# Performance work log

Hardware: AMD Instinct MI355X
Metric: run time of the kernel (lower is better)

## Reference

```python
import jax, jax.numpy as jnp
import numpy as np

# dims: B=4 batch, S=2048 seq, D=4096 in, O=4096 out, E=16 adapters, R=16 rank

def setup_inputs() -> dict:
    key = jax.random.key(0)
    k = jax.random.split(key, 6)
    x = jax.random.normal(k[0], (4, 2048, 4096), jnp.float32)
    W = jax.random.normal(k[1], (4096, 4096), jnp.float32) * 0.02   # base_linear.weight [O, D]
    bias = jax.random.normal(k[2], (4096,), jnp.float32) * 0.02
    A = jax.random.normal(k[3], (16, 16, 4096), jnp.float32) * 0.02  # stacked a_factors [E, R, D]
    Bf = jax.random.normal(k[4], (16, 4096, 16), jnp.float32) * 0.02 # stacked b_factors [E, O, R]
    coeffs = jax.random.uniform(k[5], (16,), jnp.float32)            # task coefficients per adapter
    scales = jnp.full((16,), 0.5, jnp.float32)                       # per-adapter static scales
    return {"x": x, "W": W, "bias": bias, "A": A, "Bf": Bf, "coeffs": coeffs, "scales": scales}

def reference(x, W, bias, A, Bf, coeffs, scales):
    # base: out = x @ W.T + bias
    out = jnp.einsum('bsd,od->bso', x, W) + bias
    # fused LoRA: sum_e coeffs[e]*scales[e] * (x @ A[e].T) @ Bf[e].T
    xa = jnp.einsum('bsd,erd->ebsr', x, A)          # [E, B, S, R] (small: R=16)
    w = coeffs * scales                               # [E]
    upd = jnp.einsum('ebsr,eor,e->bso', xa, Bf, w)  # weighted accumulate over adapters
    return out + upd
```

## Files before the change

### kernel.cpp

```cpp
#include <hip/hip_runtime.h>

typedef float f32x4 __attribute__((ext_vector_type(4)));
typedef __bf16 bf16x8 __attribute__((ext_vector_type(8)));
typedef unsigned short u16x8 __attribute__((ext_vector_type(8)));

__device__ __forceinline__ unsigned short f2bf(float f) {
  union { float f; unsigned int u; } v; v.f = f;
  unsigned int u = v.u;
  unsigned int r = (u + 0x7FFFu + ((u >> 16) & 1u)) >> 16;
  return (unsigned short)r;
}

__global__ __launch_bounds__(256) void k_cast_bf16(const float* __restrict__ in,
                                                   unsigned short* __restrict__ out, int n8) {
  const f32x4* p = (const f32x4*)in;
  for (int i = blockIdx.x * 256 + threadIdx.x; i < n8; i += 2048 * 256) {
    f32x4 a = p[2 * i], b = p[2 * i + 1];
    u16x8 o;
    o[0] = f2bf(a[0]); o[1] = f2bf(a[1]); o[2] = f2bf(a[2]); o[3] = f2bf(a[3]);
    o[4] = f2bf(b[0]); o[5] = f2bf(b[1]); o[6] = f2bf(b[2]); o[7] = f2bf(b[3]);
    ((u16x8*)out)[i] = o;
  }
}

__global__ void k_build_bw(const float* __restrict__ Bf,
                           const float* __restrict__ coeffs,
                           const float* __restrict__ scales,
                           unsigned short* __restrict__ bw) {
  int t = blockIdx.x * 256 + threadIdx.x;
  int o = t >> 8, k = t & 255, e = k >> 4, r = k & 15;
  float v = coeffs[e] * scales[e] * Bf[((size_t)e * 4096 + o) * 16 + r];
  bw[t] = f2bf(v);
}

__global__ void k_build_at(const float* __restrict__ A,
                           unsigned short* __restrict__ at) {
  __shared__ float tile[64][65];
  int kt = blockIdx.x * 64, dt = blockIdx.y * 64;
  int tx = threadIdx.x & 63, ty = threadIdx.x >> 6;
#pragma unroll
  for (int j = 0; j < 64; j += 4)
    tile[ty + j][tx] = A[(size_t)(kt + ty + j) * 4096 + dt + tx];
  __syncthreads();
#pragma unroll
  for (int j = 0; j < 64; j += 4)
    at[(size_t)(dt + ty + j) * 256 + kt + tx] = f2bf(tile[tx][ty + j]);
}

template <int M_, int N_, int K_>
__global__ __launch_bounds__(256) void k_gemm_prep(
    const unsigned short* __restrict__ Abuf,
    const unsigned short* __restrict__ Bbuf,
    const float* __restrict__ Wadd,
    unsigned short* __restrict__ outB) {
  constexpr int NBN = N_ / 128;
  constexpr int NWG = (M_ / 128) * NBN;
  const int bid = blockIdx.x;
  const int swz = (bid & 7) * (NWG / 8) + (bid >> 3);
  const int bm = swz / NBN, bn = swz % NBN;

  __shared__ unsigned short ldsA[128 * 64];
  __shared__ unsigned short ldsB[128 * 64];

  const int t = threadIdx.x, w = t >> 6, l = t & 63;
  const int wr = w >> 1, wc = w & 1;

  f32x4 acc[4][4] = {};
  const int m0 = bm * 128, n0 = bn * 128;
  const int srow = w * 8 + (l >> 3);
  const int scol = (l & 7) * 8;
  const unsigned short* gA = Abuf + (size_t)(m0 + srow) * K_ + scol;
  const unsigned short* gB = Bbuf + (size_t)(n0 + srow) * K_ + scol;

  for (int kt = 0; kt < K_; kt += 64) {
#pragma unroll
    for (int i = 0; i < 4; ++i) {
      __builtin_amdgcn_global_load_lds(
          (__attribute__((address_space(1))) void*)(gA + (size_t)i * 32 * K_ + kt),
          (__attribute__((address_space(3))) void*)(ldsA + i * 2048 + w * 512), 16, 0, 0);
      __builtin_amdgcn_global_load_lds(
          (__attribute__((address_space(1))) void*)(gB + (size_t)i * 32 * K_ + kt),
          (__attribute__((address_space(3))) void*)(ldsB + i * 2048 + w * 512), 16, 0, 0);
    }
    __syncthreads();
#pragma unroll
    for (int kk = 0; kk < 2; ++kk) {
      const int col = kk * 32 + (l >> 4) * 8;
      const int arow = wr * 64 + (l & 15);
      const int brow = wc * 64 + (l & 15);
      bf16x8 af[4], bfv[4];
#pragma unroll
      for (int mi = 0; mi < 4; ++mi)
        af[mi] = *(const bf16x8*)&ldsA[(arow + mi * 16) * 64 + col];
#pragma unroll
      for (int ni = 0; ni < 4; ++ni)
        bfv[ni] = *(const bf16x8*)&ldsB[(brow + ni * 16) * 64 + col];
#pragma unroll
      for (int mi = 0; mi < 4; ++mi)
#pragma unroll
        for (int ni = 0; ni < 4; ++ni)
          acc[mi][ni] = __builtin_amdgcn_mfma_f32_16x16x32_bf16(
              af[mi], bfv[ni], acc[mi][ni], 0, 0, 0);
    }
    __syncthreads();
  }

  const int mrow0 = m0 + wr * 64 + (l >> 4) * 4;
  const int ncol0 = n0 + wc * 64 + (l & 15);
#pragma unroll
  for (int mi = 0; mi < 4; ++mi)
#pragma unroll
    for (int r = 0; r < 4; ++r) {
      const int m = mrow0 + mi * 16 + r;
#pragma unroll
      for (int ni = 0; ni < 4; ++ni) {
        const int n = ncol0 + ni * 16;
        outB[(size_t)m * N_ + n] = f2bf(acc[mi][ni][r] + Wadd[(size_t)m * N_ + n]);
      }
    }
}

template <int M_, int N_, int K_>
__global__ __launch_bounds__(512, 2) void k_gemm256(
    const unsigned short* __restrict__ Abuf,
    const unsigned short* __restrict__ Bbuf,
    const float* __restrict__ bias,
    float* __restrict__ outF) {
  constexpr int NBN = N_ / 256;
  constexpr int NWG = (M_ / 256) * NBN;
  constexpr int NT = K_ / 32;
  static_assert(NWG % 8 == 0, "bijective xcd swizzle");
  static_assert(NT >= 4, "pipeline depth");

  const int bid = blockIdx.x;
  const int swz = (bid & 7) * (NWG / 8) + (bid >> 3);
  const int bm = swz / NBN, bn = swz % NBN;
  const int m0 = bm * 256, n0 = bn * 256;

  __shared__ __attribute__((aligned(128))) unsigned short lds[65536];
  char* ldsb = (char*)lds;

  const int tid = threadIdx.x, w = tid >> 6, l = tid & 63;
  const int wr = w >> 2, wc = w & 3;

  const int scol = ((l & 3) ^ ((l >> 3) & 3)) * 8;
  const unsigned short* gA = Abuf + (size_t)(m0 + w * 16 + (l >> 2)) * K_ + scol;
  const unsigned short* gB = Bbuf + (size_t)(n0 + w * 16 + (l >> 2)) * K_ + scol;
  const int dA = w * 1024;
  const int dB = 16384 + w * 1024;

  const int qp = ((l >> 4) ^ ((l >> 1) & 3)) << 4;
  const int raOff = (wr * 128 + (l & 15)) * 64 + qp;
  const int rbOff = 16384 + (wc * 64 + (l & 15)) * 64 + qp;

  f32x4 acc[8][4] = {};

#define STAGE_A(tt)                                                                   \
  do {                                                                                \
    const int bb_ = ((tt) & 3) << 15;                                                 \
    const size_t ko_ = (size_t)(tt) * 32;                                             \
    _Pragma("unroll") for (int i_ = 0; i_ < 2; ++i_) {                                \
      __builtin_amdgcn_global_load_lds(                                               \
          (__attribute__((address_space(1))) void*)(gA + (size_t)i_ * 128 * K_ + ko_),\
          (__attribute__((address_space(3))) void*)(ldsb + bb_ + i_ * 8192 + dA),     \
          16, 0, 0);                                                                  \
    }                                                                                 \
  } while (0)
#define STAGE_B(tt)                                                                   \
  do {                                                                                \
    const int bb_ = ((tt) & 3) << 15;                                                 \
    const size_t ko_ = (size_t)(tt) * 32;                                             \
    _Pragma("unroll") for (int i_ = 0; i_ < 2; ++i_) {                                \
      __builtin_amdgcn_global_load_lds(                                               \
          (__attribute__((address_space(1))) void*)(gB + (size_t)i_ * 128 * K_ + ko_),\
          (__attribute__((address_space(3))) void*)(ldsb + bb_ + i_ * 8192 + dB),     \
          16, 0, 0);                                                                  \
    }                                                                                 \
  } while (0)

  STAGE_A(0); STAGE_B(0); STAGE_A(1); STAGE_B(1); STAGE_A(2); STAGE_B(2);

  for (int t = 0; t < NT; ++t) {
    const int bb0 = (t & 3) << 15;

    if (t + 3 < NT) STAGE_A(t + 3);
    if (t + 3 < NT)      asm volatile("s_waitcnt vmcnt(10)" ::: "memory");
    else if (t + 2 < NT) asm volatile("s_waitcnt vmcnt(8)" ::: "memory");
    else if (t + 1 < NT) asm volatile("s_waitcnt vmcnt(4)" ::: "memory");
    else                 asm volatile("s_waitcnt vmcnt(0)" ::: "memory");
    __builtin_amdgcn_s_barrier();
    __builtin_amdgcn_sched_barrier(0);

    bf16x8 af[4], bv[4];
#pragma unroll
    for (int mi = 0; mi < 4; ++mi)
      af[mi] = *(const bf16x8*)(ldsb + bb0 + raOff + mi * 1024);
#pragma unroll
    for (int ni = 0; ni < 4; ++ni)
      bv[ni] = *(const bf16x8*)(ldsb + bb0 + rbOff + ni * 1024);

    __builtin_amdgcn_s_barrier();
    __builtin_amdgcn_sched_barrier(0);
    __builtin_amdgcn_s_setprio(1);
#pragma unroll
    for (int mi = 0; mi < 4; ++mi)
#pragma unroll
      for (int ni = 0; ni < 4; ++ni)
        acc[mi][ni] = __builtin_amdgcn_mfma_f32_16x16x32_bf16(
            af[mi], bv[ni], acc[mi][ni], 0, 0, 0);
    __builtin_amdgcn_s_setprio(0);

    if (t + 3 < NT) STAGE_B(t + 3);
    bf16x8 ag[4];
#pragma unroll
    for (int mi = 0; mi < 4; ++mi)
      ag[mi] = *(const bf16x8*)(ldsb + bb0 + raOff + (mi + 4) * 1024);

    __builtin_amdgcn_s_barrier();
    __builtin_amdgcn_sched_barrier(0);
    __builtin_amdgcn_s_setprio(1);
#pragma unroll
    for (int mi = 0; mi < 4; ++mi)
#pragma unroll
      for (int ni = 0; ni < 4; ++ni)
        acc[mi + 4][ni] = __builtin_amdgcn_mfma_f32_16x16x32_bf16(
            ag[mi], bv[ni], acc[mi + 4][ni], 0, 0, 0);
    __builtin_amdgcn_s_setprio(0);
  }
#undef STAGE_A
#undef STAGE_B

#pragma unroll
  for (int ni = 0; ni < 4; ++ni) {
    const int n = n0 + wc * 64 + ni * 16 + (l & 15);
    const float bv2 = bias[n];
#pragma unroll
    for (int mi = 0; mi < 8; ++mi) {
      const int m = m0 + wr * 128 + mi * 16 + (l >> 4) * 4;
#pragma unroll
      for (int r = 0; r < 4; ++r)
        outF[(size_t)(m + r) * N_ + n] = acc[mi][ni][r] + bv2;
    }
  }
}

extern "C" void kernel_launch(void* const* d_in, const int* in_sizes, int n_in,
                              void* d_out, int out_size, void* d_ws, size_t ws_size,
                              hipStream_t stream) {
  const float* x      = (const float*)d_in[0];
  const float* W      = (const float*)d_in[1];
  const float* bias   = (const float*)d_in[2];
  const float* A      = (const float*)d_in[3];
  const float* Bf     = (const float*)d_in[4];
  const float* coeffs = (const float*)d_in[5];
  const float* scales = (const float*)d_in[6];
  float* out = (float*)d_out;

  char* ws = (char*)d_ws;
  unsigned short* xb   = (unsigned short*)(ws);
  unsigned short* weff = (unsigned short*)(ws + 67108864);
  unsigned short* bw   = (unsigned short*)(ws + 67108864 + 33554432);
  unsigned short* at   = (unsigned short*)(ws + 67108864 + 33554432 + 2097152);

  k_cast_bf16<<<2048, 256, 0, stream>>>(x, xb, (8192 * 4096) / 8);
  k_build_bw<<<4096, 256, 0, stream>>>(Bf, coeffs, scales, bw);
  k_build_at<<<dim3(4, 64), 256, 0, stream>>>(A, at);
  k_gemm_prep<4096, 4096, 256><<<1024, 256, 0, stream>>>(bw, at, W, weff);
  k_gemm256<8192, 4096, 4096><<<512, 512, 0, stream>>>(xb, weff, bias, out);
}
```

Measured before the change: 359.6 us.

## Unroll GEMM k-loop by two with a five-slot LDS ring buffer

Replaces the four-slot LDS ring with a five-slot ring and processes two k-tiles per loop iteration. This allows a single barrier per pair of k-steps instead of two barriers per step. A and B stages are merged into one load macro, and LDS fragment reads for the next tile are interleaved with MFMA blocks. The aim is to cut barrier and synchronisation overhead and to improve overlap of LDS reads with matrix math. The cost is more LDS (160KB), higher register pressure from holding two tiles of fragments, and an extra requirement that NT be even.

```diff
diff --git a/kernel.cpp b/kernel.cpp
--- a/kernel.cpp
+++ b/kernel.cpp
@@ -130,14 +130,14 @@
   constexpr int NWG = (M_ / 256) * NBN;
   constexpr int NT = K_ / 32;
   static_assert(NWG % 8 == 0, "bijective xcd swizzle");
-  static_assert(NT >= 4, "pipeline depth");
+  static_assert(NT % 2 == 0 && NT >= 6, "pipeline depth");
 
   const int bid = blockIdx.x;
   const int swz = (bid & 7) * (NWG / 8) + (bid >> 3);
   const int bm = swz / NBN, bn = swz % NBN;
   const int m0 = bm * 256, n0 = bn * 256;
 
-  __shared__ __attribute__((aligned(128))) unsigned short lds[65536];
+  __shared__ __attribute__((aligned(128))) unsigned short lds[81920];
   char* ldsb = (char*)lds;
 
   const int tid = threadIdx.x, w = tid >> 6, l = tid & 63;
@@ -155,22 +155,15 @@
 
   f32x4 acc[8][4] = {};
 
-#define STAGE_A(tt)                                                                   \
+#define STAGE_T(tt, bf)                                                               \
   do {                                                                                \
-    const int bb_ = ((tt) & 3) << 15;                                                 \
+    const int bb_ = (bf) * 32768;                                                     \
     const size_t ko_ = (size_t)(tt) * 32;                                             \
     _Pragma("unroll") for (int i_ = 0; i_ < 2; ++i_) {                                \
       __builtin_amdgcn_global_load_lds(                                               \
           (__attribute__((address_space(1))) void*)(gA + (size_t)i_ * 128 * K_ + ko_),\
           (__attribute__((address_space(3))) void*)(ldsb + bb_ + i_ * 8192 + dA),     \
           16, 0, 0);                                                                  \
-    }                                                                                 \
-  } while (0)
-#define STAGE_B(tt)                                                                   \
-  do {                                                                                \
-    const int bb_ = ((tt) & 3) << 15;                                                 \
-    const size_t ko_ = (size_t)(tt) * 32;                                             \
-    _Pragma("unroll") for (int i_ = 0; i_ < 2; ++i_) {                                \
       __builtin_amdgcn_global_load_lds(                                               \
           (__attribute__((address_space(1))) void*)(gB + (size_t)i_ * 128 * K_ + ko_),\
           (__attribute__((address_space(3))) void*)(ldsb + bb_ + i_ * 8192 + dB),     \
@@ -178,57 +171,79 @@
     }                                                                                 \
   } while (0)
 
-  STAGE_A(0); STAGE_B(0); STAGE_A(1); STAGE_B(1); STAGE_A(2); STAGE_B(2);
-
-  for (int t = 0; t < NT; ++t) {
-    const int bb0 = (t & 3) << 15;
-
-    if (t + 3 < NT) STAGE_A(t + 3);
-    if (t + 3 < NT)      asm volatile("s_waitcnt vmcnt(10)" ::: "memory");
-    else if (t + 2 < NT) asm volatile("s_waitcnt vmcnt(8)" ::: "memory");
-    else if (t + 1 < NT) asm volatile("s_waitcnt vmcnt(4)" ::: "memory");
-    else                 asm volatile("s_waitcnt vmcnt(0)" ::: "memory");
+#define RD_A(mi, bf) (*(const bf16x8*)(ldsb + (bf) * 32768 + raOff + (mi) * 1024))
+#define RD_B(ni, bf) (*(const bf16x8*)(ldsb + (bf) * 32768 + rbOff + (ni) * 1024))
+
+  STAGE_T(0, 0); STAGE_T(1, 1); STAGE_T(2, 2);
+
+  int bT = 0;
+  for (int tt = 0; tt < NT; tt += 2) {
+    const int b0 = bT;
+    const int b1 = (bT + 1 >= 5) ? bT + 1 - 5 : bT + 1;
+    const int s3 = (bT + 3 >= 5) ? bT + 3 - 5 : bT + 3;
+    const int s4 = (bT + 4 >= 5) ? bT + 4 - 5 : bT + 4;
+
+    if (tt + 2 < NT) asm volatile("s_waitcnt vmcnt(4)" ::: "memory");
+    else             asm volatile("s_waitcnt vmcnt(0)" ::: "memory");
     __builtin_amdgcn_s_barrier();
     __builtin_amdgcn_sched_barrier(0);
 
-    bf16x8 af[4], bv[4];
-#pragma unroll
-    for (int mi = 0; mi < 4; ++mi)
-      af[mi] = *(const bf16x8*)(ldsb + bb0 + raOff + mi * 1024);
-#pragma unroll
-    for (int ni = 0; ni < 4; ++ni)
-      bv[ni] = *(const bf16x8*)(ldsb + bb0 + rbOff + ni * 1024);
-
-    __builtin_amdgcn_s_barrier();
-    __builtin_amdgcn_sched_barrier(0);
+    bf16x8 a0 = RD_A(0, b0), a1 = RD_A(1, b0), a2 = RD_A(2, b0), a3 = RD_A(3, b0);
+    bf16x8 v0 = RD_B(0, b0), v1 = RD_B(1, b0), v2 = RD_B(2, b0), v3 = RD_B(3, b0);
+    if (tt + 3 < NT) STAGE_T(tt + 3, s3);
+
     __builtin_amdgcn_s_setprio(1);
 #pragma unroll
-    for (int mi = 0; mi < 4; ++mi)
-#pragma unroll
-      for (int ni = 0; ni < 4; ++ni)
-        acc[mi][ni] = __builtin_amdgcn_mfma_f32_16x16x32_bf16(
-            af[mi], bv[ni], acc[mi][ni], 0, 0, 0);
+    for (int ni = 0; ni < 4; ++ni) {
+      bf16x8 vv = (ni == 0) ? v0 : (ni == 1) ? v1 : (ni == 2) ? v2 : v3;
+      acc[0][ni] = __builtin_amdgcn_mfma_f32_16x16x32_bf16(a0, vv, acc[0][ni], 0, 0, 0);
+      acc[1][ni] = __builtin_amdgcn_mfma_f32_16x16x32_bf16(a1, vv, acc[1][ni], 0, 0, 0);
+      acc[2][ni] = __builtin_amdgcn_mfma_f32_16x16x32_bf16(a2, vv, acc[2][ni], 0, 0, 0);
+      acc[3][ni] = __builtin_amdgcn_mfma_f32_16x16x32_bf16(a3, vv, acc[3][ni], 0, 0, 0);
+    }
     __builtin_amdgcn_s_setprio(0);
 
-    if (t + 3 < NT) STAGE_B(t + 3);
-    bf16x8 ag[4];
-#pragma unroll
-    for (int mi = 0; mi < 4; ++mi)
-      ag[mi] = *(const bf16x8*)(ldsb + bb0 + raOff + (mi + 4) * 1024);
-
-    __builtin_amdgcn_s_barrier();
-    __builtin_amdgcn_sched_barrier(0);
+    bf16x8 a4 = RD_A(4, b0), a5 = RD_A(5, b0), a6 = RD_A(6, b0), a7 = RD_A(7, b0);
+    bf16x8 c0 = RD_A(0, b1), c1 = RD_A(1, b1), c2 = RD_A(2, b1), c3 = RD_A(3, b1);
+    bf16x8 u0 = RD_B(0, b1), u1 = RD_B(1, b1), u2 = RD_B(2, b1), u3 = RD_B(3, b1);
+    if (tt + 4 < NT) STAGE_T(tt + 4, s4);
+
     __builtin_amdgcn_s_setprio(1);
 #pragma unroll
-    for (int mi = 0; mi < 4; ++mi)
-#pragma unroll
-      for (int ni = 0; ni < 4; ++ni)
-        acc[mi + 4][ni] = __builtin_amdgcn_mfma_f32_16x16x32_bf16(
-            ag[mi], bv[ni], acc[mi + 4][ni], 0, 0, 0);
+    for (int ni = 0; ni < 4; ++ni) {
+      bf16x8 vv = (ni == 0) ? v0 : (ni == 1) ? v1 : (ni == 2) ? v2 : v3;
+      acc[4][ni] = __builtin_amdgcn_mfma_f32_16x16x32_bf16(a4, vv, acc[4][ni], 0, 0, 0);
+      acc[5][ni] = __builtin_amdgcn_mfma_f32_16x16x32_bf16(a5, vv, acc[5][ni], 0, 0, 0);
+      acc[6][ni] = __builtin_amdgcn_mfma_f32_16x16x32_bf16(a6, vv, acc[6][ni], 0, 0, 0);
+      acc[7][ni] = __builtin_amdgcn_mfma_f32_16x16x32_bf16(a7, vv, acc[7][ni], 0, 0, 0);
+    }
+#pragma unroll
+    for (int ni = 0; ni < 4; ++ni) {
+      bf16x8 uu = (ni == 0) ? u0 : (ni == 1) ? u1 : (ni == 2) ? u2 : u3;
+      acc[0][ni] = __builtin_amdgcn_mfma_f32_16x16x32_bf16(c0, uu, acc[0][ni], 0, 0, 0);
+      acc[1][ni] = __builtin_amdgcn_mfma_f32_16x16x32_bf16(c1, uu, acc[1][ni], 0, 0, 0);
+      acc[2][ni] = __builtin_amdgcn_mfma_f32_16x16x32_bf16(c2, uu, acc[2][ni], 0, 0, 0);
+      acc[3][ni] = __builtin_amdgcn_mfma_f32_16x16x32_bf16(c3, uu, acc[3][ni], 0, 0, 0);
+    }
     __builtin_amdgcn_s_setprio(0);
-  }
-#undef STAGE_A
-#undef STAGE_B
+
+    bf16x8 c4 = RD_A(4, b1), c5 = RD_A(5, b1), c6 = RD_A(6, b1), c7 = RD_A(7, b1);
+    __builtin_amdgcn_s_setprio(1);
+#pragma unroll
+    for (int ni = 0; ni < 4; ++ni) {
+      bf16x8 uu = (ni == 0) ? u0 : (ni == 1) ? u1 : (ni == 2) ? u2 : u3;
+      acc[4][ni] = __builtin_amdgcn_mfma_f32_16x16x32_bf16(c4, uu, acc[4][ni], 0, 0, 0);
+      acc[5][ni] = __builtin_amdgcn_mfma_f32_16x16x32_bf16(c5, uu, acc[5][ni], 0, 0, 0);
+      acc[6][ni] = __builtin_amdgcn_mfma_f32_16x16x32_bf16(c6, uu, acc[6][ni], 0, 0, 0);
+      acc[7][ni] = __builtin_amdgcn_mfma_f32_16x16x32_bf16(c7, uu, acc[7][ni], 0, 0, 0);
+    }
+    __builtin_amdgcn_s_setprio(0);
+
+    bT += 2; if (bT >= 5) bT -= 5;
+  }
+#undef STAGE_T
+#undef RD_A
+#undef RD_B
 
 #pragma unroll
   for (int ni = 0; ni < 4; ++ni) {
```

Result: faster. 346.8 us (-3.6%).
